# Optimization experiments

Hardware: AMD Instinct MI355X
Metric: run time of the kernel (lower is better)

## Reference

```python
import jax, jax.numpy as jnp
import numpy as np

UNITS = 64
T = 100


def setup_inputs() -> dict:
    key = jax.random.key(0)
    ks = jax.random.split(key, 9)
    B, F = 16384, 3
    x = jax.random.normal(ks[0], (B, T, F), dtype=jnp.float32)
    # give each sequence a random valid length; zero the tail so Masking(0.0) kicks in
    lengths = jax.random.randint(ks[8], (B,), 20, T + 1)
    valid = (jnp.arange(T)[None, :] < lengths[:, None])  # (B, T) bool
    x = x * valid[:, :, None].astype(jnp.float32)
    s = 1.0 / np.sqrt(UNITS)
    return {
        "x": x,
        "W": jax.random.normal(ks[1], (F, 4 * UNITS), dtype=jnp.float32) * s,
        "U": jax.random.normal(ks[2], (UNITS, 4 * UNITS), dtype=jnp.float32) * s,
        "b": jax.random.normal(ks[3], (4 * UNITS,), dtype=jnp.float32) * 0.1,
        "W1": jax.random.normal(ks[4], (UNITS, 64), dtype=jnp.float32) * s,
        "b1": jnp.zeros((64,), dtype=jnp.float32),
        "W2": jax.random.normal(ks[5], (64, 5), dtype=jnp.float32) * s,
        "b2": jnp.zeros((5,), dtype=jnp.float32),
    }


def _masked_lstm(x, W, U, b):
    # x: (B, T, F). Keras Masking(0.0): step masked iff all features == 0.
    B = x.shape[0]
    mask = jnp.any(x != 0.0, axis=-1)                 # (B, T)
    xT = jnp.swapaxes(x, 0, 1)                        # (T, B, F)
    mT = jnp.swapaxes(mask, 0, 1)                     # (T, B)
    # precompute input projection for all steps: (T, B, 4U)
    zx = jnp.einsum('tbf,fg->tbg', xT, W) + b
    h0 = jnp.zeros((B, UNITS), dtype=x.dtype)
    c0 = jnp.zeros((B, UNITS), dtype=x.dtype)

    def step(carry, inp):
        h, c = carry
        zxt, mt = inp
        z = zxt + h @ U                               # (B, 4U)
        i, f, g, o = jnp.split(z, 4, axis=-1)         # Keras gate order i,f,c,o
        i = jax.nn.sigmoid(i)
        f = jax.nn.sigmoid(f)
        o = jax.nn.sigmoid(o)
        c_new = f * c + i * jnp.tanh(g)
        h_new = o * jnp.tanh(c_new)
        m = mt[:, None]
        h = jnp.where(m, h_new, h)                    # masked steps: carry state
        c = jnp.where(m, c_new, c)
        return (h, c), None

    (h, _), _ = jax.lax.scan(step, (h0, c0), (zx, mT))
    return h                                          # (B, UNITS) last carried output


def reference(x, W, U, b, W1, b1, W2, b2):
    h = _masked_lstm(x, W, U, b)
    h1 = jax.nn.relu(h @ W1 + b1)
    return jax.nn.softmax(h1 @ W2 + b2, axis=-1)      # (B, 5)
```

## Files before the change

kernel.cpp:

```cpp
#include <hip/hip_runtime.h>
#include <math.h>

#define UNITS 64
#define TT 100
#define NB 16
#define NTH 256
#define HSTR 72
#define XQSTR 18

typedef _Float16 half8 __attribute__((ext_vector_type(8)));
typedef _Float16 half4 __attribute__((ext_vector_type(4)));
typedef float floatx4 __attribute__((ext_vector_type(4)));

#define LOG2E 1.44269504088896f

__device__ __forceinline__ float rcp_fast(float x) { return __builtin_amdgcn_rcpf(x); }
__device__ __forceinline__ float exp2_fast(float x) { return __builtin_amdgcn_exp2f(x); }

__device__ __forceinline__ float fast_sigmoid(float x) {
    return rcp_fast(1.0f + exp2_fast(-LOG2E * x));
}
__device__ __forceinline__ float fast_tanh(float x) {
    return __builtin_fmaf(2.0f, rcp_fast(1.0f + exp2_fast(-2.0f * LOG2E * x)), -1.0f);
}

__global__ __launch_bounds__(NTH, 4) void lstm_kernel(
    const float* __restrict__ x,
    const float* __restrict__ W,
    const float* __restrict__ U,
    const float* __restrict__ bias,
    const float* __restrict__ W1,
    const float* __restrict__ b1,
    const float* __restrict__ W2,
    const float* __restrict__ b2,
    float* __restrict__ out, int B)
{
    __shared__ __align__(16) _Float16 hb[2][NB * HSTR];
    __shared__ __align__(16) _Float16 xt[TT * XQSTR * 4];
    __shared__ __align__(16) _Float16 zq[8];
    __shared__ int llen_s[NB];
    __shared__ float h1buf[NB * 64];
    __shared__ float logitbuf[NB * 5];

    const int tid = threadIdx.x;
    const int w   = tid >> 6;
    const int l   = tid & 63;
    const int q   = l >> 4;
    const int cnl = l & 15;
    const int b0  = blockIdx.x * NB;
    const int grp = tid >> 4;
    const int sub = tid & 15;

    {
        const float* xp = x + (size_t)(b0 + grp) * (TT * 3);
        int m = 0;
        for (int t = sub; t < TT; t += 16) {
            const float a = xp[3*t], b = xp[3*t+1], c = xp[3*t+2];
            if (a != 0.0f || b != 0.0f || c != 0.0f) m = t + 1;
        }
        #pragma unroll
        for (int off = 8; off; off >>= 1) m = max(m, __shfl_down(m, off, 16));
        if (sub == 0) llen_s[grp] = m;
    }
    if (tid < 8) zq[tid] = (_Float16)0.0f;
    for (int i = tid; i < NB * HSTR; i += NTH) hb[0][i] = (_Float16)0.0f;
    __syncthreads();

    int maxlen = 0, minlen = TT;
    #pragma unroll
    for (int i = 0; i < NB; ++i) {
        const int v = llen_s[i];
        maxlen = max(maxlen, v);
        minlen = min(minlen, v);
    }
    maxlen = (maxlen < 0) ? 0 : ((maxlen > TT) ? TT : maxlen);
    minlen = (minlen < 0) ? 0 : ((minlen > maxlen) ? maxlen : minlen);
    int rl[4];
    #pragma unroll
    for (int r = 0; r < 4; ++r) rl[r] = llen_s[4*q + r];

    {
        const float* xp = x + (size_t)(b0 + grp) * (TT * 3);
        for (int t = sub; t < maxlen; t += 16) {
            const float a = xp[3*t], b = xp[3*t+1], c = xp[3*t+2];
            half4 v = { (_Float16)a, (_Float16)b, (_Float16)c, (_Float16)1.0f };
            *(half4*)&xt[(t * XQSTR + grp) * 4] = v;
        }
    }

    half8 Bf[4][3];
    #pragma unroll
    for (int g = 0; g < 4; ++g) {
        const int zc = 64 * g + 16 * w + cnl;
        #pragma unroll
        for (int kb = 0; kb < 3; ++kb)
            #pragma unroll
            for (int j = 0; j < 8; ++j) {
                const int k = 32 * kb + 8 * q + j;
                float v = 0.0f;
                if (k < 64)       v = U[k * 256 + zc];
                else if (k < 67)  v = W[(k - 64) * 256 + zc];
                else if (k == 67) v = bias[zc];
                Bf[g][kb][j] = (_Float16)v;
            }
    }

    float c4[4] = {0.0f, 0.0f, 0.0f, 0.0f};
    _Float16 hcur[4] = {(_Float16)0.0f, (_Float16)0.0f, (_Float16)0.0f, (_Float16)0.0f};
    const floatx4 zero4 = {0.0f, 0.0f, 0.0f, 0.0f};

    __syncthreads();

    int t = 0;

    #pragma unroll 1
    for (; t < minlen; ++t) {
        const _Float16* hbc = hb[t & 1];
        _Float16*       hbn = hb[(t + 1) & 1];

        const half8 A0 = *(const half8*)&hbc[cnl * HSTR + 8 * q];
        const half8 A1 = *(const half8*)&hbc[cnl * HSTR + 32 + 8 * q];
        const _Float16* xaddr = (q == 0) ? &xt[(t * XQSTR + cnl) * 4] : zq;
        const half4 x4 = *(const half4*)xaddr;
        const half8 AX = { x4[0], x4[1], x4[2], x4[3],
                           (_Float16)0.0f, (_Float16)0.0f, (_Float16)0.0f, (_Float16)0.0f };

        floatx4 acc[4];
        #pragma unroll
        for (int g = 0; g < 4; ++g) {
            acc[g] = __builtin_amdgcn_mfma_f32_16x16x32_f16(AX, Bf[g][2], zero4, 0, 0, 0);
            acc[g] = __builtin_amdgcn_mfma_f32_16x16x32_f16(A0, Bf[g][0], acc[g], 0, 0, 0);
            acc[g] = __builtin_amdgcn_mfma_f32_16x16x32_f16(A1, Bf[g][1], acc[g], 0, 0, 0);
        }

        #pragma unroll
        for (int r = 0; r < 4; ++r) {
            const float iv = fast_sigmoid(acc[0][r]);
            const float fv = fast_sigmoid(acc[1][r]);
            const float gv = fast_tanh  (acc[2][r]);
            const float ov = fast_sigmoid(acc[3][r]);
            const float cn = fv * c4[r] + iv * gv;
            c4[r] = cn;
            hcur[r] = (_Float16)(ov * fast_tanh(cn));
            hbn[(4 * q + r) * HSTR + 16 * w + cnl] = hcur[r];
        }
        __syncthreads();
    }

    #pragma unroll 1
    for (; t < maxlen; ++t) {
        const _Float16* hbc = hb[t & 1];
        _Float16*       hbn = hb[(t + 1) & 1];

        const half8 A0 = *(const half8*)&hbc[cnl * HSTR + 8 * q];
        const half8 A1 = *(const half8*)&hbc[cnl * HSTR + 32 + 8 * q];
        const _Float16* xaddr = (q == 0) ? &xt[(t * XQSTR + cnl) * 4] : zq;
        const half4 x4 = *(const half4*)xaddr;
        const half8 AX = { x4[0], x4[1], x4[2], x4[3],
                           (_Float16)0.0f, (_Float16)0.0f, (_Float16)0.0f, (_Float16)0.0f };

        floatx4 acc[4];
        #pragma unroll
        for (int g = 0; g < 4; ++g) {
            acc[g] = __builtin_amdgcn_mfma_f32_16x16x32_f16(AX, Bf[g][2], zero4, 0, 0, 0);
            acc[g] = __builtin_amdgcn_mfma_f32_16x16x32_f16(A0, Bf[g][0], acc[g], 0, 0, 0);
            acc[g] = __builtin_amdgcn_mfma_f32_16x16x32_f16(A1, Bf[g][1], acc[g], 0, 0, 0);
        }

        #pragma unroll
        for (int r = 0; r < 4; ++r) {
            const bool live = (t < rl[r]);
            const float iv = fast_sigmoid(acc[0][r]);
            const float fv = fast_sigmoid(acc[1][r]);
            const float gv = fast_tanh  (acc[2][r]);
            const float ov = fast_sigmoid(acc[3][r]);
            const float cn = fv * c4[r] + iv * gv;
            c4[r] = live ? cn : c4[r];
            const _Float16 hn = (_Float16)(ov * fast_tanh(cn));
            hcur[r] = live ? hn : hcur[r];
            hbn[(4 * q + r) * HSTR + 16 * w + cnl] = hcur[r];
        }
        __syncthreads();
    }

    const _Float16* hbL = hb[maxlen & 1];

    {
        const int j  = tid & 63;
        const int bb = tid >> 6;
        const float bj = b1[j];
        #pragma unroll
        for (int p = 0; p < NB / 4; ++p) {
            const int b = p * 4 + bb;
            float acc = bj;
            #pragma unroll 8
            for (int k = 0; k < UNITS; ++k)
                acc += (float)hbL[b * HSTR + k] * W1[k * 64 + j];
            h1buf[b * 64 + j] = fmaxf(acc, 0.0f);
        }
    }
    __syncthreads();

    if (tid < NB * 5) {
        const int b = tid / 5, s = tid % 5;
        float acc = b2[s];
        for (int j = 0; j < 64; ++j)
            acc += h1buf[b * 64 + j] * W2[j * 5 + s];
        logitbuf[b * 5 + s] = acc;
    }
    __syncthreads();

    if (tid < NB) {
        const int gb = b0 + tid;
        const float l0 = logitbuf[tid * 5 + 0];
        const float l1 = logitbuf[tid * 5 + 1];
        const float l2 = logitbuf[tid * 5 + 2];
        const float l3 = logitbuf[tid * 5 + 3];
        const float l4 = logitbuf[tid * 5 + 4];
        const float m  = fmaxf(fmaxf(fmaxf(l0, l1), fmaxf(l2, l3)), l4);
        const float e0 = __expf(l0 - m), e1 = __expf(l1 - m), e2 = __expf(l2 - m);
        const float e3 = __expf(l3 - m), e4 = __expf(l4 - m);
        const float rs = 1.0f / (e0 + e1 + e2 + e3 + e4);
        out[(size_t)gb * 5 + 0] = e0 * rs;
        out[(size_t)gb * 5 + 1] = e1 * rs;
        out[(size_t)gb * 5 + 2] = e2 * rs;
        out[(size_t)gb * 5 + 3] = e3 * rs;
        out[(size_t)gb * 5 + 4] = e4 * rs;
    }
}

extern "C" void kernel_launch(void* const* d_in, const int* in_sizes, int n_in,
                              void* d_out, int out_size, void* d_ws, size_t ws_size,
                              hipStream_t stream) {
    const float* x  = (const float*)d_in[0];
    const float* W  = (const float*)d_in[1];
    const float* U  = (const float*)d_in[2];
    const float* b  = (const float*)d_in[3];
    const float* W1 = (const float*)d_in[4];
    const float* b1 = (const float*)d_in[5];
    const float* W2 = (const float*)d_in[6];
    const float* b2 = (const float*)d_in[7];
    float* out = (float*)d_out;

    const int B = in_sizes[0] / (TT * 3);

    lstm_kernel<<<dim3(B / NB), dim3(NTH), 0, stream>>>(
        x, W, U, b, W1, b1, W2, b2, out, B);
}
```

Baseline: 213.9 us.

## Pack sorted variable-length sequences in pairs into shared LSTM slots

Each block now handles 32 sequences instead of 16. It sorts them by valid length and pairs the longest with the shortest, so each of the 16 MFMA row slots runs two sequences back to back. At a sequence boundary the carried h and c are reset and the final hidden state goes to a separate buffer. This cuts the recurrent steps wasted on masked padding, but each block now runs more steps. Launch bounds drop to 2 waves per EU, the x staging buffer in LDS grows, and the grid has half as many blocks, which may lower latency hiding in this serial loop.

```diff
diff --git a/kernel.cpp b/kernel.cpp
--- a/kernel.cpp
+++ b/kernel.cpp
@@ -3,10 +3,11 @@
 
 #define UNITS 64
 #define TT 100
-#define NB 16
+#define NROW 32
+#define NSLOT 16
 #define NTH 256
 #define HSTR 72
-#define XQSTR 18
+#define XQS 34
 
 typedef _Float16 half8 __attribute__((ext_vector_type(8)));
 typedef _Float16 half4 __attribute__((ext_vector_type(4)));
@@ -24,7 +25,7 @@
     return __builtin_fmaf(2.0f, rcp_fast(1.0f + exp2_fast(-2.0f * LOG2E * x)), -1.0f);
 }
 
-__global__ __launch_bounds__(NTH, 4) void lstm_kernel(
+__global__ __launch_bounds__(NTH, 2) void lstm_packed_kernel(
     const float* __restrict__ x,
     const float* __restrict__ W,
     const float* __restrict__ U,
@@ -35,58 +36,40 @@
     const float* __restrict__ b2,
     float* __restrict__ out, int B)
 {
-    __shared__ __align__(16) _Float16 hb[2][NB * HSTR];
-    __shared__ __align__(16) _Float16 xt[TT * XQSTR * 4];
+    __shared__ __align__(16) _Float16 hb[2][NSLOT * HSTR];
+    __shared__ __align__(16) _Float16 xq[TT * XQS * 4];
+    __shared__ __align__(16) _Float16 hfin[NROW * HSTR];
     __shared__ __align__(16) _Float16 zq[8];
-    __shared__ int llen_s[NB];
-    __shared__ float h1buf[NB * 64];
-    __shared__ float logitbuf[NB * 5];
+    __shared__ int llen_s[NROW];
+    __shared__ int sortedIdx[NROW];
+    __shared__ int slotA[NSLOT], slotB[NSLOT], slotLA[NSLOT], slotTL[NSLOT];
+    __shared__ float h1buf[NROW * 64];
+    __shared__ float logitbuf[NROW * 5];
 
     const int tid = threadIdx.x;
     const int w   = tid >> 6;
     const int l   = tid & 63;
     const int q   = l >> 4;
     const int cnl = l & 15;
-    const int b0  = blockIdx.x * NB;
-    const int grp = tid >> 4;
-    const int sub = tid & 15;
+    const int g0  = blockIdx.x * NROW;
+    const int rower = tid >> 3;
+    const int s8    = tid & 7;
 
     {
-        const float* xp = x + (size_t)(b0 + grp) * (TT * 3);
+        const float* xp = x + (size_t)(g0 + rower) * (TT * 3);
         int m = 0;
-        for (int t = sub; t < TT; t += 16) {
+        for (int t = s8; t < TT; t += 8) {
             const float a = xp[3*t], b = xp[3*t+1], c = xp[3*t+2];
             if (a != 0.0f || b != 0.0f || c != 0.0f) m = t + 1;
         }
         #pragma unroll
-        for (int off = 8; off; off >>= 1) m = max(m, __shfl_down(m, off, 16));
-        if (sub == 0) llen_s[grp] = m;
+        for (int off = 4; off; off >>= 1) m = max(m, __shfl_down(m, off, 8));
+        if (s8 == 0) llen_s[rower] = m;
     }
     if (tid < 8) zq[tid] = (_Float16)0.0f;
-    for (int i = tid; i < NB * HSTR; i += NTH) hb[0][i] = (_Float16)0.0f;
-    __syncthreads();
-
-    int maxlen = 0, minlen = TT;
-    #pragma unroll
-    for (int i = 0; i < NB; ++i) {
-        const int v = llen_s[i];
-        maxlen = max(maxlen, v);
-        minlen = min(minlen, v);
-    }
-    maxlen = (maxlen < 0) ? 0 : ((maxlen > TT) ? TT : maxlen);
-    minlen = (minlen < 0) ? 0 : ((minlen > maxlen) ? maxlen : minlen);
-    int rl[4];
-    #pragma unroll
-    for (int r = 0; r < 4; ++r) rl[r] = llen_s[4*q + r];
-
-    {
-        const float* xp = x + (size_t)(b0 + grp) * (TT * 3);
-        for (int t = sub; t < maxlen; t += 16) {
-            const float a = xp[3*t], b = xp[3*t+1], c = xp[3*t+2];
-            half4 v = { (_Float16)a, (_Float16)b, (_Float16)c, (_Float16)1.0f };
-            *(half4*)&xt[(t * XQSTR + grp) * 4] = v;
-        }
-    }
+    for (int i = tid; i < NSLOT * HSTR; i += NTH) hb[0][i] = (_Float16)0.0f;
+    for (int i = tid; i < NROW * HSTR; i += NTH) hfin[i] = (_Float16)0.0f;
+    for (int i = tid; i < TT * XQS * 4; i += NTH) xq[i] = (_Float16)0.0f;
 
     half8 Bf[4][3];
     #pragma unroll
@@ -105,22 +88,67 @@
             }
     }
 
+    __syncthreads();
+
+    if (tid < NROW) {
+        const int li = llen_s[tid];
+        int rank = 0;
+        for (int j = 0; j < NROW; ++j) {
+            const int lj = llen_s[j];
+            rank += (lj > li) || (lj == li && j < tid);
+        }
+        sortedIdx[rank] = tid;
+    }
+    __syncthreads();
+    if (tid < NSLOT) {
+        const int a = sortedIdx[tid];
+        const int b = sortedIdx[NROW - 1 - tid];
+        slotA[tid] = a; slotB[tid] = b;
+        const int la = llen_s[a];
+        slotLA[tid] = la;
+        slotTL[tid] = la + llen_s[b];
+    }
+    {
+        const float* xp = x + (size_t)(g0 + rower) * (TT * 3);
+        const int myl = llen_s[rower];
+        for (int t = s8; t < myl; t += 8) {
+            half4 v = { (_Float16)xp[3*t], (_Float16)xp[3*t+1],
+                        (_Float16)xp[3*t+2], (_Float16)1.0f };
+            *(half4*)&xq[(t * XQS + rower) * 4] = v;
+        }
+    }
+    __syncthreads();
+
+    int lAr[4], TLr[4], rAr[4], rBr[4];
+    #pragma unroll
+    for (int r = 0; r < 4; ++r) {
+        const int s = 4 * q + r;
+        lAr[r] = slotLA[s]; TLr[r] = slotTL[s];
+        rAr[r] = slotA[s];  rBr[r] = slotB[s];
+    }
+    const int xsLA = slotLA[cnl], xsRowA = slotA[cnl], xsRowB = slotB[cnl];
+    int maxstep = 0;
+    #pragma unroll
+    for (int i = 0; i < NSLOT; ++i) maxstep = max(maxstep, slotTL[i]);
+    maxstep = (maxstep < 0) ? 0 : ((maxstep > 2 * TT) ? 2 * TT : maxstep);
+
     float c4[4] = {0.0f, 0.0f, 0.0f, 0.0f};
     _Float16 hcur[4] = {(_Float16)0.0f, (_Float16)0.0f, (_Float16)0.0f, (_Float16)0.0f};
     const floatx4 zero4 = {0.0f, 0.0f, 0.0f, 0.0f};
-
-    __syncthreads();
-
-    int t = 0;
+    const int col = 16 * w + cnl;
 
     #pragma unroll 1
-    for (; t < minlen; ++t) {
+    for (int t = 0; t < maxstep; ++t) {
         const _Float16* hbc = hb[t & 1];
         _Float16*       hbn = hb[(t + 1) & 1];
 
         const half8 A0 = *(const half8*)&hbc[cnl * HSTR + 8 * q];
         const half8 A1 = *(const half8*)&hbc[cnl * HSTR + 32 + 8 * q];
-        const _Float16* xaddr = (q == 0) ? &xt[(t * XQSTR + cnl) * 4] : zq;
+        const int inA  = (t < xsLA);
+        const int xrow = inA ? xsRowA : xsRowB;
+        int tl = inA ? t : (t - xsLA);
+        tl = (tl > TT - 1) ? (TT - 1) : tl;
+        const _Float16* xaddr = (q == 0) ? &xq[(tl * XQS + xrow) * 4] : zq;
         const half4 x4 = *(const half4*)xaddr;
         const half8 AX = { x4[0], x4[1], x4[2], x4[3],
                            (_Float16)0.0f, (_Float16)0.0f, (_Float16)0.0f, (_Float16)0.0f };
@@ -140,68 +168,35 @@
             const float gv = fast_tanh  (acc[2][r]);
             const float ov = fast_sigmoid(acc[3][r]);
             const float cn = fv * c4[r] + iv * gv;
-            c4[r] = cn;
-            hcur[r] = (_Float16)(ov * fast_tanh(cn));
-            hbn[(4 * q + r) * HSTR + 16 * w + cnl] = hcur[r];
+            const _Float16 hn = (_Float16)(ov * fast_tanh(cn));
+            const bool aEnd = (t == lAr[r] - 1);
+            const bool bEnd = (t == TLr[r] - 1);
+            if (aEnd) hfin[rAr[r] * HSTR + col] = hn;
+            if (bEnd) hfin[rBr[r] * HSTR + col] = hn;
+            c4[r]   = aEnd ? 0.0f : cn;
+            hcur[r] = aEnd ? (_Float16)0.0f : hn;
+            hbn[(4 * q + r) * HSTR + col] = hcur[r];
         }
         __syncthreads();
     }
-
-    #pragma unroll 1
-    for (; t < maxlen; ++t) {
-        const _Float16* hbc = hb[t & 1];
-        _Float16*       hbn = hb[(t + 1) & 1];
-
-        const half8 A0 = *(const half8*)&hbc[cnl * HSTR + 8 * q];
-        const half8 A1 = *(const half8*)&hbc[cnl * HSTR + 32 + 8 * q];
-        const _Float16* xaddr = (q == 0) ? &xt[(t * XQSTR + cnl) * 4] : zq;
-        const half4 x4 = *(const half4*)xaddr;
-        const half8 AX = { x4[0], x4[1], x4[2], x4[3],
-                           (_Float16)0.0f, (_Float16)0.0f, (_Float16)0.0f, (_Float16)0.0f };
-
-        floatx4 acc[4];
-        #pragma unroll
-        for (int g = 0; g < 4; ++g) {
-            acc[g] = __builtin_amdgcn_mfma_f32_16x16x32_f16(AX, Bf[g][2], zero4, 0, 0, 0);
-            acc[g] = __builtin_amdgcn_mfma_f32_16x16x32_f16(A0, Bf[g][0], acc[g], 0, 0, 0);
-            acc[g] = __builtin_amdgcn_mfma_f32_16x16x32_f16(A1, Bf[g][1], acc[g], 0, 0, 0);
-        }
-
-        #pragma unroll
-        for (int r = 0; r < 4; ++r) {
-            const bool live = (t < rl[r]);
-            const float iv = fast_sigmoid(acc[0][r]);
-            const float fv = fast_sigmoid(acc[1][r]);
-            const float gv = fast_tanh  (acc[2][r]);
-            const float ov = fast_sigmoid(acc[3][r]);
-            const float cn = fv * c4[r] + iv * gv;
-            c4[r] = live ? cn : c4[r];
-            const _Float16 hn = (_Float16)(ov * fast_tanh(cn));
-            hcur[r] = live ? hn : hcur[r];
-            hbn[(4 * q + r) * HSTR + 16 * w + cnl] = hcur[r];
-        }
-        __syncthreads();
-    }
-
-    const _Float16* hbL = hb[maxlen & 1];
 
     {
         const int j  = tid & 63;
         const int bb = tid >> 6;
         const float bj = b1[j];
         #pragma unroll
-        for (int p = 0; p < NB / 4; ++p) {
+        for (int p = 0; p < NROW / 4; ++p) {
             const int b = p * 4 + bb;
             float acc = bj;
             #pragma unroll 8
             for (int k = 0; k < UNITS; ++k)
-                acc += (float)hbL[b * HSTR + k] * W1[k * 64 + j];
+                acc += (float)hfin[b * HSTR + k] * W1[k * 64 + j];
             h1buf[b * 64 + j] = fmaxf(acc, 0.0f);
         }
     }
     __syncthreads();
 
-    if (tid < NB * 5) {
+    if (tid < NROW * 5) {
         const int b = tid / 5, s = tid % 5;
         float acc = b2[s];
         for (int j = 0; j < 64; ++j)
@@ -210,8 +205,8 @@
     }
     __syncthreads();
 
-    if (tid < NB) {
-        const int gb = b0 + tid;
+    if (tid < NROW) {
+        const int gb = g0 + tid;
         const float l0 = logitbuf[tid * 5 + 0];
         const float l1 = logitbuf[tid * 5 + 1];
         const float l2 = logitbuf[tid * 5 + 2];
@@ -244,6 +239,6 @@
 
     const int B = in_sizes[0] / (TT * 3);
 
-    lstm_kernel<<<dim3(B / NB), dim3(NTH), 0, stream>>>(
+    lstm_packed_kernel<<<dim3(B / NROW), dim3(NTH), 0, stream>>>(
         x, W, U, b, W1, b1, W2, b2, out, B);
 }
```

New measurement: 227.5 us. 1.06x slower.
